# Performance work log

Hardware: AMD Instinct MI355X
Metric: run time of the kernel (lower is better)

Reference implementation:

```python
import jax, jax.numpy as jnp
import numpy as np

D = 768  # hidden dim hard-coded in the module


def setup_inputs() -> dict:
    key = jax.random.key(0)
    k1, k2, k3, k4, k5 = jax.random.split(key, 5)
    N, M = 512, 512
    return {
        "text_output": jax.random.normal(k1, (N, D), dtype=jnp.float32),
        "visual_output": jax.random.normal(k2, (M, D), dtype=jnp.float32),
        "W1": jax.random.normal(k3, (D, D), dtype=jnp.float32),
        "W2": jax.random.normal(k4, (D, D), dtype=jnp.float32),
        "W3": jax.random.normal(k5, (D, D), dtype=jnp.float32),
    }


def reference(text_output, visual_output, W1, W2, W3):
    # C[n,m] = tanh( (text @ W1) . visual[m] )
    C = jnp.tanh((text_output @ W1) @ visual_output.T)            # (N, M)
    W2_text = text_output @ W2                                    # (N, D)
    W3_visual = visual_output @ W3.T                              # (M, D)
    # M[n,m,:] = tanh(W2_text[n] + W3_visual[m] * C[n,m])
    Mt = jnp.tanh(W2_text[:, None, :] + W3_visual[None, :, :] * C[..., None])  # (N, M, D)
    # score[n,m] = text[n] . M[n,m]  (replaces the per-row Python loop)
    score = jnp.einsum("nd,nmd->nm", text_output, Mt)             # (N, M)
    return score
```

## Files before the change

kernel.cpp:

```cpp
#include <hip/hip_runtime.h>

#define DD   768
#define NN   512
#define MM   512

#define PRE_K 2.88539008177792681472f

typedef _Float16 h8 __attribute__((ext_vector_type(8)));
typedef __attribute__((ext_vector_type(4))) float f32x4;

__device__ __forceinline__ float fexp(float x) { return __builtin_amdgcn_exp2f(x); }
__device__ __forceinline__ float frcp(float x) { return __builtin_amdgcn_rcpf(x); }
__device__ __forceinline__ float fast_tanh(float x) {
  return 1.0f - 2.0f * frcp(fexp(PRE_K * x) + 1.0f);
}

__device__ __forceinline__ void splitf(float x, ushort& h, ushort& l) {
  const _Float16 hh = (_Float16)x;
  const _Float16 ll = (_Float16)(x - (float)hh);
  h = __builtin_bit_cast(unsigned short, hh);
  l = __builtin_bit_cast(unsigned short, ll);
}

__global__ __launch_bounds__(256) void convert_kernel(
    const float* __restrict__ text, const float* __restrict__ visual,
    const float* __restrict__ W3,
    ushort* __restrict__ th, ushort* __restrict__ tl,
    ushort* __restrict__ vh, ushort* __restrict__ vl,
    ushort* __restrict__ w3h, ushort* __restrict__ w3l)
{
  const int z = blockIdx.z;
  const float* src = (z == 0) ? text : (z == 1) ? visual : W3;
  ushort* dh = (z == 0) ? th : (z == 1) ? vh : w3h;
  ushort* dl = (z == 0) ? tl : (z == 1) ? vl : w3l;
  const int count = ((z == 2) ? DD * DD : NN * DD) / 4;
  const int i = blockIdx.x * 256 + threadIdx.x;
  if (i >= count) return;
  const float4 v = *(const float4*)&src[(size_t)i * 4];
  ushort4 h, l;
  splitf(v.x, h.x, l.x); splitf(v.y, h.y, l.y);
  splitf(v.z, h.z, l.z); splitf(v.w, h.w, l.w);
  *(ushort4*)&dh[(size_t)i * 4] = h;
  *(ushort4*)&dl[(size_t)i * 4] = l;
}

__global__ __launch_bounds__(256) void transpose_kernel(
    const float* __restrict__ W1, const float* __restrict__ W2,
    ushort* __restrict__ w1th, ushort* __restrict__ w1tl,
    ushort* __restrict__ w2th, ushort* __restrict__ w2tl)
{
  __shared__ float Lt[32][33];
  const float* W = blockIdx.z ? W2 : W1;
  ushort* oh = blockIdx.z ? w2th : w1th;
  ushort* ol = blockIdx.z ? w2tl : w1tl;
  const int k0 = blockIdx.y * 32, j0 = blockIdx.x * 32;
  const int t = threadIdx.x;
  {
    const int k = t >> 3, j4 = (t & 7) * 4;
    const float4 v = *(const float4*)&W[(size_t)(k0 + k) * DD + j0 + j4];
    Lt[j4 + 0][k] = v.x; Lt[j4 + 1][k] = v.y;
    Lt[j4 + 2][k] = v.z; Lt[j4 + 3][k] = v.w;
  }
  __syncthreads();
  {
    const int j = t >> 3, k4 = (t & 7) * 4;
    ushort4 h, l;
    splitf(Lt[j][k4 + 0], h.x, l.x); splitf(Lt[j][k4 + 1], h.y, l.y);
    splitf(Lt[j][k4 + 2], h.z, l.z); splitf(Lt[j][k4 + 3], h.w, l.w);
    *(ushort4*)&oh[(size_t)(j0 + j) * DD + k0 + k4] = h;
    *(ushort4*)&ol[(size_t)(j0 + j) * DD + k0 + k4] = l;
  }
}

#define BK   32
#define LROW 40

__device__ __forceinline__ void gemm_core(
    const ushort* __restrict__ Ahg, const ushort* __restrict__ Alg,
    const ushort* __restrict__ Bhg, const ushort* __restrict__ Blg,
    int i0, int j0, int k0, int nsteps, f32x4* acc)
{
  __shared__ ushort As[2][2][64 * LROW];
  __shared__ ushort Bs[2][2][64 * LROW];

  const int tid  = threadIdx.x;
  const int row  = tid >> 2;
  const int ks8  = (tid & 3) * 8;
  const size_t ga = (size_t)(i0 + row) * DD + k0 + ks8;
  const size_t gb = (size_t)(j0 + row) * DD + k0 + ks8;
  const int ldsw = row * LROW + ks8;

  const int lane = tid & 63, wave = tid >> 6;
  const int r15 = lane & 15, quad = lane >> 4;
  const int fa = (wave * 16 + r15) * LROW + quad * 8;
  const int fb = r15 * LROW + quad * 8;

  h8 pah = *(const h8*)(Ahg + ga);
  h8 pal = *(const h8*)(Alg + ga);
  h8 pbh = *(const h8*)(Bhg + gb);
  h8 pbl = *(const h8*)(Blg + gb);

  int p = 0;
  *(h8*)&As[0][0][ldsw] = pah; *(h8*)&As[0][1][ldsw] = pal;
  *(h8*)&Bs[0][0][ldsw] = pbh; *(h8*)&Bs[0][1][ldsw] = pbl;
  __syncthreads();

  for (int s = 0; s < nsteps; ++s) {
    const bool more = (s + 1 < nsteps);
    if (more) {
      pah = *(const h8*)(Ahg + ga + (s + 1) * BK);
      pal = *(const h8*)(Alg + ga + (s + 1) * BK);
      pbh = *(const h8*)(Bhg + gb + (s + 1) * BK);
      pbl = *(const h8*)(Blg + gb + (s + 1) * BK);
    }
    const h8 a_h = *(const h8*)&As[p][0][fa];
    const h8 a_l = *(const h8*)&As[p][1][fa];
    h8 b_h[4], b_l[4];
    #pragma unroll
    for (int c = 0; c < 4; ++c) {
      b_h[c] = *(const h8*)&Bs[p][0][fb + c * 16 * LROW];
      b_l[c] = *(const h8*)&Bs[p][1][fb + c * 16 * LROW];
    }
    #pragma unroll
    for (int c = 0; c < 4; ++c)
      acc[c] = __builtin_amdgcn_mfma_f32_16x16x32_f16(a_h, b_h[c], acc[c], 0, 0, 0);
    #pragma unroll
    for (int c = 0; c < 4; ++c)
      acc[c] = __builtin_amdgcn_mfma_f32_16x16x32_f16(a_h, b_l[c], acc[c], 0, 0, 0);
    #pragma unroll
    for (int c = 0; c < 4; ++c)
      acc[c] = __builtin_amdgcn_mfma_f32_16x16x32_f16(a_l, b_h[c], acc[c], 0, 0, 0);
    if (more) {
      const int q = p ^ 1;
      *(h8*)&As[q][0][ldsw] = pah; *(h8*)&As[q][1][ldsw] = pal;
      *(h8*)&Bs[q][0][ldsw] = pbh; *(h8*)&Bs[q][1][ldsw] = pbl;
    }
    __syncthreads();
    p ^= 1;
  }
}

__global__ __launch_bounds__(256) void mfma1_kernel(
    const ushort* __restrict__ th, const ushort* __restrict__ tl,
    const ushort* __restrict__ vh, const ushort* __restrict__ vl,
    const ushort* __restrict__ w1th, const ushort* __restrict__ w1tl,
    const ushort* __restrict__ w2th, const ushort* __restrict__ w2tl,
    const ushort* __restrict__ w3h, const ushort* __restrict__ w3l,
    ushort* __restrict__ Ah, ushort* __restrict__ Al,
    float* __restrict__ kw2t, float* __restrict__ kw3v)
{
  const int z  = blockIdx.z;
  const int j0 = blockIdx.x * 64;
  const int i0 = blockIdx.y * 64;
  const ushort *Arh, *Arl, *Brh, *Brl;
  if (z == 0)      { Arh = th; Arl = tl; Brh = w1th; Brl = w1tl; }
  else if (z == 1) { Arh = th; Arl = tl; Brh = w2th; Brl = w2tl; }
  else             { Arh = vh; Arl = vl; Brh = w3h;  Brl = w3l;  }

  f32x4 acc[4];
  #pragma unroll
  for (int c = 0; c < 4; ++c) acc[c] = (f32x4){0.f, 0.f, 0.f, 0.f};
  gemm_core(Arh, Arl, Brh, Brl, i0, j0, 0, DD / BK, acc);

  const int lane = threadIdx.x & 63, wave = threadIdx.x >> 6;
  const int r15 = lane & 15, quad = lane >> 4;
  if (z == 0) {
    #pragma unroll
    for (int c = 0; c < 4; ++c)
      #pragma unroll
      for (int r = 0; r < 4; ++r) {
        const size_t o = (size_t)(i0 + wave * 16 + quad * 4 + r) * DD + j0 + c * 16 + r15;
        splitf(acc[c][r], Ah[o], Al[o]);
      }
  } else {
    float* Out = (z == 1) ? kw2t : kw3v;
    #pragma unroll
    for (int c = 0; c < 4; ++c)
      #pragma unroll
      for (int r = 0; r < 4; ++r)
        Out[(size_t)(i0 + wave * 16 + quad * 4 + r) * DD + j0 + c * 16 + r15] =
            acc[c][r] * PRE_K;
  }
}

__global__ __launch_bounds__(256) void mfma2_kernel(
    const ushort* __restrict__ Ah, const ushort* __restrict__ Al,
    const ushort* __restrict__ vh, const ushort* __restrict__ vl,
    float* __restrict__ Q)
{
  const int z  = blockIdx.z;
  const int j0 = blockIdx.x * 64;
  const int i0 = blockIdx.y * 64;

  f32x4 acc[4];
  #pragma unroll
  for (int c = 0; c < 4; ++c) acc[c] = (f32x4){0.f, 0.f, 0.f, 0.f};
  gemm_core(Ah, Al, vh, vl, i0, j0, z * (DD / 2), (DD / 2) / BK, acc);

  const int lane = threadIdx.x & 63, wave = threadIdx.x >> 6;
  const int r15 = lane & 15, quad = lane >> 4;
  float* Out = Q + (size_t)z * NN * MM;
  #pragma unroll
  for (int c = 0; c < 4; ++c)
    #pragma unroll
    for (int r = 0; r < 4; ++r)
      Out[(size_t)(i0 + wave * 16 + quad * 4 + r) * MM + j0 + c * 16 + r15] = acc[c][r];
}

__global__ __launch_bounds__(256) void reducec_kernel(
    const float* __restrict__ Q, float* __restrict__ Ct)
{
  const size_t i = ((size_t)blockIdx.x * 256 + threadIdx.x) * 4;
  const float4 q0 = *(const float4*)&Q[i];
  const float4 q1 = *(const float4*)&Q[(size_t)NN * MM + i];
  float4 o;
  o.x = fast_tanh(q0.x + q1.x); o.y = fast_tanh(q0.y + q1.y);
  o.z = fast_tanh(q0.z + q1.z); o.w = fast_tanh(q0.w + q1.w);
  *(float4*)&Ct[i] = o;
}

__global__ __launch_bounds__(64) void tsum_kernel(
    const float* __restrict__ text, float* __restrict__ T)
{
  const int n = blockIdx.x;
  const int lane = threadIdx.x;
  float s = 0.f;
  #pragma unroll
  for (int i = 0; i < DD / 64; ++i) s += text[n * DD + lane + i * 64];
  #pragma unroll
  for (int off = 32; off; off >>= 1) s += __shfl_down(s, off);
  if (lane == 0) T[n] = s;
}

#define DCH    64
#define DRANGE 256
#define MLDW   68

__global__ __launch_bounds__(256) void main_kernel(
    const float* __restrict__ text, const float* __restrict__ kw2t,
    const float* __restrict__ kw3v, const float* __restrict__ Ct,
    float* __restrict__ Spart)
{
  __shared__ float ts[16][MLDW];
  __shared__ float w2s[16][MLDW];
  __shared__ float w3s[32][MLDW];

  const int tid = threadIdx.x;
  const int nl = tid >> 4;
  const int ml = tid & 15;
  const int n0 = blockIdx.y * 16;
  const int m0 = blockIdx.x * 32;
  const int z  = blockIdx.z;
  const int n  = n0 + nl;
  const int mA = m0 + ml, mB = mA + 16;
  const int dbase = z * DRANGE;

  const float cA = Ct[(size_t)n * MM + mA];
  const float cB = Ct[(size_t)n * MM + mB];

  float4 aA = {0.f, 0.f, 0.f, 0.f};
  float4 aB = {0.f, 0.f, 0.f, 0.f};

  const int srow = tid >> 4;
  const int sc4  = (tid & 15) << 2;

  for (int dc = 0; dc < DRANGE; dc += DCH) {
    const int d0 = dbase + dc;
    *(float4*)&ts[srow][sc4]       = *(const float4*)&text[(size_t)(n0 + srow) * DD + d0 + sc4];
    *(float4*)&w2s[srow][sc4]      = *(const float4*)&kw2t[(size_t)(n0 + srow) * DD + d0 + sc4];
    *(float4*)&w3s[srow][sc4]      = *(const float4*)&kw3v[(size_t)(m0 + srow) * DD + d0 + sc4];
    *(float4*)&w3s[srow + 16][sc4] = *(const float4*)&kw3v[(size_t)(m0 + 16 + srow) * DD + d0 + sc4];
    __syncthreads();

    #pragma unroll 4
    for (int j = 0; j < DCH; j += 4) {
      const float4 tv  = *(const float4*)&ts[nl][j];
      const float4 w2  = *(const float4*)&w2s[nl][j];
      const float4 w3A = *(const float4*)&w3s[ml][j];
      const float4 w3B = *(const float4*)&w3s[ml + 16][j];
      aA.x = fmaf(tv.x, frcp(fexp(fmaf(w3A.x, cA, w2.x)) + 1.0f), aA.x);
      aA.y = fmaf(tv.y, frcp(fexp(fmaf(w3A.y, cA, w2.y)) + 1.0f), aA.y);
      aA.z = fmaf(tv.z, frcp(fexp(fmaf(w3A.z, cA, w2.z)) + 1.0f), aA.z);
      aA.w = fmaf(tv.w, frcp(fexp(fmaf(w3A.w, cA, w2.w)) + 1.0f), aA.w);
      aB.x = fmaf(tv.x, frcp(fexp(fmaf(w3B.x, cB, w2.x)) + 1.0f), aB.x);
      aB.y = fmaf(tv.y, frcp(fexp(fmaf(w3B.y, cB, w2.y)) + 1.0f), aB.y);
      aB.z = fmaf(tv.z, frcp(fexp(fmaf(w3B.z, cB, w2.z)) + 1.0f), aB.z);
      aB.w = fmaf(tv.w, frcp(fexp(fmaf(w3B.w, cB, w2.w)) + 1.0f), aB.w);
    }
    __syncthreads();
  }

  float* Sp = Spart + (size_t)z * NN * MM + (size_t)n * MM;
  Sp[mA] = (aA.x + aA.y) + (aA.z + aA.w);
  Sp[mB] = (aB.x + aB.y) + (aB.z + aB.w);
}

__global__ __launch_bounds__(256) void combine_kernel(
    const float* __restrict__ Spart, const float* __restrict__ T,
    float* __restrict__ out)
{
  const size_t i = ((size_t)blockIdx.x * 256 + threadIdx.x) * 4;
  const size_t S = (size_t)NN * MM;
  const int n = (int)(i >> 9);
  const float Tn = T[n];
  const float4 s0 = *(const float4*)&Spart[i];
  const float4 s1 = *(const float4*)&Spart[S + i];
  const float4 s2 = *(const float4*)&Spart[2 * S + i];
  float4 o;
  o.x = Tn - 2.0f * (s0.x + s1.x + s2.x);
  o.y = Tn - 2.0f * (s0.y + s1.y + s2.y);
  o.z = Tn - 2.0f * (s0.z + s1.z + s2.z);
  o.w = Tn - 2.0f * (s0.w + s1.w + s2.w);
  *(float4*)&out[i] = o;
}

extern "C" void kernel_launch(void* const* d_in, const int* in_sizes, int n_in,
                              void* d_out, int out_size, void* d_ws, size_t ws_size,
                              hipStream_t stream) {
  const float* text   = (const float*)d_in[0];
  const float* visual = (const float*)d_in[1];
  const float* W1     = (const float*)d_in[2];
  const float* W2     = (const float*)d_in[3];
  const float* W3     = (const float*)d_in[4];
  float* out = (float*)d_out;

  char* base = (char*)d_ws;
  ushort* th   = (ushort*)(base);
  ushort* tl   = (ushort*)(base + 786432);
  ushort* vh   = (ushort*)(base + 1572864);
  ushort* vl   = (ushort*)(base + 2359296);
  ushort* w1th = (ushort*)(base + 3145728);
  ushort* w1tl = (ushort*)(base + 4325376);
  ushort* w2th = (ushort*)(base + 5505024);
  ushort* w2tl = (ushort*)(base + 6684672);
  ushort* w3h  = (ushort*)(base + 7864320);
  ushort* w3l  = (ushort*)(base + 9043968);
  ushort* Ah   = (ushort*)(base + 10223616);
  ushort* Al   = (ushort*)(base + 11010048);
  float*  kw2t = (float*) (base + 11796480);
  float*  kw3v = (float*) (base + 13369344);
  float*  T    = (float*) (base + 14942208);
  float*  Q     = (float*)(base + 3145728);
  float*  Ct    = (float*)(base + 5505024);
  float*  Spart = (float*)(base + 6684672);

  hipLaunchKernelGGL(tsum_kernel, dim3(NN), dim3(64), 0, stream, text, T);
  hipLaunchKernelGGL(convert_kernel, dim3(DD * DD / 1024, 1, 3), dim3(256), 0, stream,
                     text, visual, W3, th, tl, vh, vl, w3h, w3l);
  hipLaunchKernelGGL(transpose_kernel, dim3(DD / 32, DD / 32, 2), dim3(256), 0, stream,
                     W1, W2, w1th, w1tl, w2th, w2tl);
  hipLaunchKernelGGL(mfma1_kernel, dim3(DD / 64, NN / 64, 3), dim3(256), 0, stream,
                     th, tl, vh, vl, w1th, w1tl, w2th, w2tl, w3h, w3l,
                     Ah, Al, kw2t, kw3v);
  hipLaunchKernelGGL(mfma2_kernel, dim3(MM / 64, NN / 64, 2), dim3(256), 0, stream,
                     Ah, Al, vh, vl, Q);
  hipLaunchKernelGGL(reducec_kernel, dim3(NN * MM / 1024), dim3(256), 0, stream,
                     Q, Ct);
  hipLaunchKernelGGL(main_kernel, dim3(MM / 32, NN / 16, 3), dim3(256), 0, stream,
                     text, kw2t, kw3v, Ct, Spart);
  hipLaunchKernelGGL(combine_kernel, dim3(NN * MM / 1024), dim3(256), 0, stream,
                     Spart, T, out);
}
```

Before: 146.7 us.

## Fuse prep kernels, fold C reduction into main and row sums into combine

Merges the convert and transpose launches into one prep kernel that dispatches on a flat block index. Drops the separate reduce-C and text-sum kernels: main_kernel now sums the split-K partials of Q and applies tanh itself, and combine_kernel computes each row's text sum with a shared-memory reduction. mfma2 is split four ways along K instead of two, giving more blocks for the small GEMM. Intent is fewer launches and fewer intermediate global round-trips, at the cost of extra Q reads in main_kernel and a larger Q workspace.

```diff
diff --git a/kernel.cpp b/kernel.cpp
--- a/kernel.cpp
+++ b/kernel.cpp
@@ -22,53 +22,55 @@
   l = __builtin_bit_cast(unsigned short, ll);
 }
 
-__global__ __launch_bounds__(256) void convert_kernel(
+__global__ __launch_bounds__(256) void prep_kernel(
     const float* __restrict__ text, const float* __restrict__ visual,
+    const float* __restrict__ W1, const float* __restrict__ W2,
     const float* __restrict__ W3,
     ushort* __restrict__ th, ushort* __restrict__ tl,
     ushort* __restrict__ vh, ushort* __restrict__ vl,
-    ushort* __restrict__ w3h, ushort* __restrict__ w3l)
-{
-  const int z = blockIdx.z;
-  const float* src = (z == 0) ? text : (z == 1) ? visual : W3;
-  ushort* dh = (z == 0) ? th : (z == 1) ? vh : w3h;
-  ushort* dl = (z == 0) ? tl : (z == 1) ? vl : w3l;
-  const int count = ((z == 2) ? DD * DD : NN * DD) / 4;
-  const int i = blockIdx.x * 256 + threadIdx.x;
-  if (i >= count) return;
-  const float4 v = *(const float4*)&src[(size_t)i * 4];
-  ushort4 h, l;
-  splitf(v.x, h.x, l.x); splitf(v.y, h.y, l.y);
-  splitf(v.z, h.z, l.z); splitf(v.w, h.w, l.w);
-  *(ushort4*)&dh[(size_t)i * 4] = h;
-  *(ushort4*)&dl[(size_t)i * 4] = l;
-}
-
-__global__ __launch_bounds__(256) void transpose_kernel(
-    const float* __restrict__ W1, const float* __restrict__ W2,
+    ushort* __restrict__ w3h, ushort* __restrict__ w3l,
     ushort* __restrict__ w1th, ushort* __restrict__ w1tl,
     ushort* __restrict__ w2th, ushort* __restrict__ w2tl)
 {
   __shared__ float Lt[32][33];
-  const float* W = blockIdx.z ? W2 : W1;
-  ushort* oh = blockIdx.z ? w2th : w1th;
-  ushort* ol = blockIdx.z ? w2tl : w1tl;
-  const int k0 = blockIdx.y * 32, j0 = blockIdx.x * 32;
+  const int b = blockIdx.x;
   const int t = threadIdx.x;
-  {
-    const int k = t >> 3, j4 = (t & 7) * 4;
-    const float4 v = *(const float4*)&W[(size_t)(k0 + k) * DD + j0 + j4];
-    Lt[j4 + 0][k] = v.x; Lt[j4 + 1][k] = v.y;
-    Lt[j4 + 2][k] = v.z; Lt[j4 + 3][k] = v.w;
-  }
-  __syncthreads();
-  {
-    const int j = t >> 3, k4 = (t & 7) * 4;
+
+  if (b < 1344) {
+    const float* src; ushort *dh, *dl; size_t off;
+    if (b < 384)      { src = text;   dh = th;  dl = tl;  off = (size_t)b * 1024; }
+    else if (b < 768) { src = visual; dh = vh;  dl = vl;  off = (size_t)(b - 384) * 1024; }
+    else              { src = W3;     dh = w3h; dl = w3l; off = (size_t)(b - 768) * 1024; }
+    const size_t i = off + (size_t)t * 4;
+    const float4 v = *(const float4*)&src[i];
     ushort4 h, l;
-    splitf(Lt[j][k4 + 0], h.x, l.x); splitf(Lt[j][k4 + 1], h.y, l.y);
-    splitf(Lt[j][k4 + 2], h.z, l.z); splitf(Lt[j][k4 + 3], h.w, l.w);
-    *(ushort4*)&oh[(size_t)(j0 + j) * DD + k0 + k4] = h;
-    *(ushort4*)&ol[(size_t)(j0 + j) * DD + k0 + k4] = l;
+    splitf(v.x, h.x, l.x); splitf(v.y, h.y, l.y);
+    splitf(v.z, h.z, l.z); splitf(v.w, h.w, l.w);
+    *(ushort4*)&dh[i] = h;
+    *(ushort4*)&dl[i] = l;
+  } else {
+    const int tt = b - 1344;
+    const bool second = tt >= 576;
+    const int tile = second ? tt - 576 : tt;
+    const float* W = second ? W2 : W1;
+    ushort* oh = second ? w2th : w1th;
+    ushort* ol = second ? w2tl : w1tl;
+    const int k0 = (tile / 24) * 32, j0 = (tile % 24) * 32;
+    {
+      const int k = t >> 3, j4 = (t & 7) * 4;
+      const float4 v = *(const float4*)&W[(size_t)(k0 + k) * DD + j0 + j4];
+      Lt[j4 + 0][k] = v.x; Lt[j4 + 1][k] = v.y;
+      Lt[j4 + 2][k] = v.z; Lt[j4 + 3][k] = v.w;
+    }
+    __syncthreads();
+    {
+      const int j = t >> 3, k4 = (t & 7) * 4;
+      ushort4 h, l;
+      splitf(Lt[j][k4 + 0], h.x, l.x); splitf(Lt[j][k4 + 1], h.y, l.y);
+      splitf(Lt[j][k4 + 2], h.z, l.z); splitf(Lt[j][k4 + 3], h.w, l.w);
+      *(ushort4*)&oh[(size_t)(j0 + j) * DD + k0 + k4] = h;
+      *(ushort4*)&ol[(size_t)(j0 + j) * DD + k0 + k4] = l;
+    }
   }
 }
 
@@ -195,7 +197,7 @@
   f32x4 acc[4];
   #pragma unroll
   for (int c = 0; c < 4; ++c) acc[c] = (f32x4){0.f, 0.f, 0.f, 0.f};
-  gemm_core(Ah, Al, vh, vl, i0, j0, z * (DD / 2), (DD / 2) / BK, acc);
+  gemm_core(Ah, Al, vh, vl, i0, j0, z * (DD / 4), (DD / 4) / BK, acc);
 
   const int lane = threadIdx.x & 63, wave = threadIdx.x >> 6;
   const int r15 = lane & 15, quad = lane >> 4;
@@ -207,38 +209,13 @@
       Out[(size_t)(i0 + wave * 16 + quad * 4 + r) * MM + j0 + c * 16 + r15] = acc[c][r];
 }
 
-__global__ __launch_bounds__(256) void reducec_kernel(
-    const float* __restrict__ Q, float* __restrict__ Ct)
-{
-  const size_t i = ((size_t)blockIdx.x * 256 + threadIdx.x) * 4;
-  const float4 q0 = *(const float4*)&Q[i];
-  const float4 q1 = *(const float4*)&Q[(size_t)NN * MM + i];
-  float4 o;
-  o.x = fast_tanh(q0.x + q1.x); o.y = fast_tanh(q0.y + q1.y);
-  o.z = fast_tanh(q0.z + q1.z); o.w = fast_tanh(q0.w + q1.w);
-  *(float4*)&Ct[i] = o;
-}
-
-__global__ __launch_bounds__(64) void tsum_kernel(
-    const float* __restrict__ text, float* __restrict__ T)
-{
-  const int n = blockIdx.x;
-  const int lane = threadIdx.x;
-  float s = 0.f;
-  #pragma unroll
-  for (int i = 0; i < DD / 64; ++i) s += text[n * DD + lane + i * 64];
-  #pragma unroll
-  for (int off = 32; off; off >>= 1) s += __shfl_down(s, off);
-  if (lane == 0) T[n] = s;
-}
-
 #define DCH    64
 #define DRANGE 256
 #define MLDW   68
 
 __global__ __launch_bounds__(256) void main_kernel(
     const float* __restrict__ text, const float* __restrict__ kw2t,
-    const float* __restrict__ kw3v, const float* __restrict__ Ct,
+    const float* __restrict__ kw3v, const float* __restrict__ Q,
     float* __restrict__ Spart)
 {
   __shared__ float ts[16][MLDW];
@@ -255,8 +232,13 @@
   const int mA = m0 + ml, mB = mA + 16;
   const int dbase = z * DRANGE;
 
-  const float cA = Ct[(size_t)n * MM + mA];
-  const float cB = Ct[(size_t)n * MM + mB];
+  float cA = 0.f, cB = 0.f;
+  #pragma unroll
+  for (int zz = 0; zz < 4; ++zz) {
+    const float* q = Q + (size_t)zz * NN * MM + (size_t)n * MM;
+    cA += q[mA]; cB += q[mB];
+  }
+  cA = fast_tanh(cA); cB = fast_tanh(cB);
 
   float4 aA = {0.f, 0.f, 0.f, 0.f};
   float4 aB = {0.f, 0.f, 0.f, 0.f};
@@ -296,13 +278,33 @@
 }
 
 __global__ __launch_bounds__(256) void combine_kernel(
-    const float* __restrict__ Spart, const float* __restrict__ T,
+    const float* __restrict__ Spart, const float* __restrict__ text,
     float* __restrict__ out)
 {
-  const size_t i = ((size_t)blockIdx.x * 256 + threadIdx.x) * 4;
+  __shared__ float red[256];
+  __shared__ float Tsh[2];
+  const int b = blockIdx.x, t = threadIdx.x;
+  const int n0 = b * 2;
+  const int half = t >> 7;
+  const int lt = t & 127;
+
+  const float* tr = text + (size_t)(n0 + half) * DD;
+  float s = 0.f;
+  #pragma unroll
+  for (int i = 0; i < DD / 128; ++i) s += tr[lt + i * 128];
+  red[t] = s;
+  __syncthreads();
+  #pragma unroll
+  for (int st = 64; st > 0; st >>= 1) {
+    if (lt < st) red[t] += red[t + st];
+    __syncthreads();
+  }
+  if (lt == 0) Tsh[half] = red[t];
+  __syncthreads();
+
+  const size_t i = (size_t)b * 1024 + (size_t)t * 4;
   const size_t S = (size_t)NN * MM;
-  const int n = (int)(i >> 9);
-  const float Tn = T[n];
+  const float Tn = Tsh[half];
   const float4 s0 = *(const float4*)&Spart[i];
   const float4 s1 = *(const float4*)&Spart[S + i];
   const float4 s2 = *(const float4*)&Spart[2 * S + i];
@@ -339,25 +341,19 @@
   ushort* Al   = (ushort*)(base + 11010048);
   float*  kw2t = (float*) (base + 11796480);
   float*  kw3v = (float*) (base + 13369344);
-  float*  T    = (float*) (base + 14942208);
   float*  Q     = (float*)(base + 3145728);
-  float*  Ct    = (float*)(base + 5505024);
-  float*  Spart = (float*)(base + 6684672);
-
-  hipLaunchKernelGGL(tsum_kernel, dim3(NN), dim3(64), 0, stream, text, T);
-  hipLaunchKernelGGL(convert_kernel, dim3(DD * DD / 1024, 1, 3), dim3(256), 0, stream,
-                     text, visual, W3, th, tl, vh, vl, w3h, w3l);
-  hipLaunchKernelGGL(transpose_kernel, dim3(DD / 32, DD / 32, 2), dim3(256), 0, stream,
-                     W1, W2, w1th, w1tl, w2th, w2tl);
+  float*  Spart = (float*)(base + 7864320);
+
+  hipLaunchKernelGGL(prep_kernel, dim3(2496), dim3(256), 0, stream,
+                     text, visual, W1, W2, W3,
+                     th, tl, vh, vl, w3h, w3l, w1th, w1tl, w2th, w2tl);
   hipLaunchKernelGGL(mfma1_kernel, dim3(DD / 64, NN / 64, 3), dim3(256), 0, stream,
                      th, tl, vh, vl, w1th, w1tl, w2th, w2tl, w3h, w3l,
                      Ah, Al, kw2t, kw3v);
-  hipLaunchKernelGGL(mfma2_kernel, dim3(MM / 64, NN / 64, 2), dim3(256), 0, stream,
+  hipLaunchKernelGGL(mfma2_kernel, dim3(MM / 64, NN / 64, 4), dim3(256), 0, stream,
                      Ah, Al, vh, vl, Q);
-  hipLaunchKernelGGL(reducec_kernel, dim3(NN * MM / 1024), dim3(256), 0, stream,
-                     Q, Ct);
   hipLaunchKernelGGL(main_kernel, dim3(MM / 32, NN / 16, 3), dim3(256), 0, stream,
-                     text, kw2t, kw3v, Ct, Spart);
+                     text, kw2t, kw3v, Q, Spart);
   hipLaunchKernelGGL(combine_kernel, dim3(NN * MM / 1024), dim3(256), 0, stream,
-                     Spart, T, out);
-}
+                     Spart, text, out);
+}
```

Result: faster. 140.5 us (-4.3%).
